# Optimization experiments

Hardware: AMD Instinct MI355X
Metric: run time of the kernel (lower is better)

## Reference

```python
import jax, jax.numpy as jnp
import numpy as np

WIN = 25            # window size (win_h == win_w == 25)
DIM = 256           # channels
DIM_HEAD = 32
HEADS = DIM // DIM_HEAD   # 8
HIDDEN = int(DIM * 2.0)   # mlp_ratio = 2.0
EPS = 1e-5


def _rel_pos_indices(w=WIN):
    # replicates the buffer built in Attention.__init__
    pos = np.arange(w)
    gi, gj = np.meshgrid(pos, pos, indexing='ij')
    grid = np.stack([gi.ravel(), gj.ravel()], axis=-1)          # (w*w, 2)
    rel = grid[:, None, :] - grid[None, :, :] + (w - 1)          # (n, n, 2)
    return jnp.asarray(rel[..., 0] * (2 * w - 1) + rel[..., 1])  # (n, n) int


def setup_inputs() -> dict:
    key = jax.random.key(0)
    ks = jax.random.split(key, 8)
    s = 0.02
    d = DIM
    return {
        'x': jax.random.normal(ks[0], (2, d, 100, 100), jnp.float32),
        'w_qkv': jax.random.normal(ks[1], (3 * d, d), jnp.float32) * s,
        'w_out': jax.random.normal(ks[2], (d, d), jnp.float32) * s,
        'rel_bias_table': jax.random.normal(ks[3], ((2 * WIN - 1) ** 2, HEADS), jnp.float32) * s,
        'gamma2': jnp.ones((d,), jnp.float32),
        'beta2': jnp.zeros((d,), jnp.float32),
        'w1': jax.random.normal(ks[4], (HIDDEN, d), jnp.float32) * s,
        'b1': jnp.zeros((HIDDEN,), jnp.float32),
        'w2': jax.random.normal(ks[5], (d, HIDDEN), jnp.float32) * s,
        'b2': jnp.zeros((d,), jnp.float32),
    }


def _layernorm(x, g, b, eps=EPS):
    m = x.mean(-1, keepdims=True)
    v = ((x - m) ** 2).mean(-1, keepdims=True)
    return (x - m) / jnp.sqrt(v + eps) * g + b


def reference(x, w_qkv, w_out, rel_bias_table, gamma2, beta2, w1, b1, w2, b2):
    b, d, H, W = x.shape
    nh, nw = H // WIN, W // WIN
    h, dh = HEADS, DIM_HEAD
    scale = dh ** -0.5
    n = WIN * WIN

    # --- window partition: (b, d, H, W) -> (b*nh*nw, n, d) ---
    xw = x.reshape(b, d, nh, WIN, nw, WIN).transpose(0, 2, 4, 3, 5, 1)
    xw = xw.reshape(b * nh * nw, n, d)

    # --- windowed attention with relative-position bias (norm1 unused in source) ---
    qkv = xw @ w_qkv.T                         # (B, n, 3d)
    q, k, v = jnp.split(qkv, 3, axis=-1)
    split_heads = lambda t: t.reshape(t.shape[0], n, h, dh).transpose(0, 2, 1, 3)
    q = split_heads(q) * scale                 # (B, h, n, dh)
    k = split_heads(k)
    v = split_heads(v)

    sim = jnp.einsum('bhid,bhjd->bhij', q, k)  # (B, h, n, n)
    bias = rel_bias_table[_rel_pos_indices()]  # (n, n, h)
    sim = sim + bias.transpose(2, 0, 1)[None]
    attn = jax.nn.softmax(sim, axis=-1)
    out = jnp.einsum('bhij,bhjd->bhid', attn, v)            # (B, h, n, dh)
    out = out.transpose(0, 2, 1, 3).reshape(-1, n, d)        # head-major concat: (m d)
    out = out @ w_out.T                                      # (B, n, d)

    # --- un-partition: (b*nh*nw, n, d) -> (b, d, H, W) ---
    xa = out.reshape(b, nh, nw, WIN, WIN, d).transpose(0, 5, 1, 3, 2, 4)
    xa = xa.reshape(b, d, H, W)

    # --- norm2 + MLP + residual ---
    y = xa.transpose(0, 2, 3, 1).reshape(b, H * W, d)
    y = _layernorm(y, gamma2, beta2)
    y = jax.nn.gelu(y @ w1.T + b1, approximate=False) @ w2.T + b2
    y = y.reshape(b, H, W, d).transpose(0, 3, 1, 2)
    return x + y
```

## Files before the change

kernel.cpp:

```cpp
#include <hip/hip_runtime.h>


using f32x4 = __attribute__((ext_vector_type(4))) float;
using s16x8 = __attribute__((ext_vector_type(8))) short;
using u32x4 = __attribute__((ext_vector_type(4))) unsigned;

__device__ __forceinline__ ushort f2b(float f) {
  union { float f; unsigned u; } v; v.f = f;
  return (ushort)((v.u + 0x7FFFu + ((v.u >> 16) & 1u)) >> 16);
}
__device__ __forceinline__ ushort f2b_fast(float f) {
  union { float f; unsigned u; } v; v.f = f;
  return (ushort)((v.u + 0x8000u) >> 16);
}
__device__ __forceinline__ float b2f(ushort u) {
  union { unsigned u; float f; } v; v.u = ((unsigned)u) << 16; return v.f;
}
__device__ __forceinline__ float lo2f(unsigned w) {
  union { unsigned u; float f; } v; v.u = w << 16; return v.f;
}
__device__ __forceinline__ float hi2f(unsigned w) {
  union { unsigned u; float f; } v; v.u = w & 0xffff0000u; return v.f;
}

__device__ __forceinline__ unsigned cvtpk(float lo, float hi) {
  unsigned r;
  asm("v_cvt_pk_bf16_f32 %0, %1, %2" : "=v"(r) : "v"(lo), "v"(hi));
  return r;
}
__device__ __forceinline__ void pl32(unsigned& a, unsigned& b) {
  asm("v_permlane32_swap_b32 %0, %1" : "+v"(a), "+v"(b));
}
__device__ __forceinline__ void pl16(unsigned& a, unsigned& b) {
  asm("v_permlane16_swap_b32 %0, %1" : "+v"(a), "+v"(b));
}

__device__ __forceinline__ void gld16(const void* g, void* l) {
  __builtin_amdgcn_global_load_lds((const __attribute__((address_space(1))) void*)g,
                                   (__attribute__((address_space(3))) void*)l, 16, 0, 0);
}

template<int KB, int WM, int WN, int MT, int NT>
__device__ __forceinline__ void gemm_core(const ushort* __restrict__ A, int lda,
                                          const ushort* __restrict__ B, int ldb,
                                          f32x4 acc[MT][NT]) {
  constexpr int TM = WM * MT * 16;
  constexpr int TN = WN * NT * 16;
  constexpr int NW = WM * WN;
  constexpr int RG = (TM + TN) / 8;
  static_assert(NW == 4 && RG % NW == 0 && TM % 8 == 0, "cfg");
  __shared__ ushort As[TM * 64];
  __shared__ ushort Bs[TN * 64];
  const int tid = threadIdx.x;
  const int lane = tid & 63;
  const int wv = tid >> 6;
  const int wr = (wv / WN) * (MT * 16);
  const int wc = (wv % WN) * (NT * 16);
  const int srow = lane >> 3;
  const int sg = ((lane & 7) ^ (srow & 7)) * 8;
  f32x4 zero = {0.f, 0.f, 0.f, 0.f};
#pragma unroll
  for (int mt = 0; mt < MT; ++mt)
#pragma unroll
    for (int nt = 0; nt < NT; ++nt) acc[mt][nt] = zero;

  for (int kb = 0; kb < KB; ++kb) {
#pragma unroll
    for (int i = 0; i < RG / NW; ++i) {
      int r0 = (i * NW + wv) * 8;
      if (r0 < TM) gld16(A + (r0 + srow) * lda + kb * 64 + sg, &As[r0 * 64]);
      else         gld16(B + (r0 - TM + srow) * ldb + kb * 64 + sg, &Bs[(r0 - TM) * 64]);
    }
    __syncthreads();
#pragma unroll
    for (int ks = 0; ks < 2; ++ks) {
      s16x8 af[MT], bfr[NT];
      const int G = ks * 4 + (lane >> 4);
#pragma unroll
      for (int mt = 0; mt < MT; ++mt) {
        int row = wr + mt * 16 + (lane & 15);
        af[mt] = *(const s16x8*)&As[row * 64 + (G ^ (row & 7)) * 8];
      }
#pragma unroll
      for (int nt = 0; nt < NT; ++nt) {
        int row = wc + nt * 16 + (lane & 15);
        bfr[nt] = *(const s16x8*)&Bs[row * 64 + (G ^ (row & 7)) * 8];
      }
#pragma unroll
      for (int mt = 0; mt < MT; ++mt)
#pragma unroll
        for (int nt = 0; nt < NT; ++nt)
          acc[mt][nt] = __builtin_amdgcn_mfma_f32_16x16x32_bf16(af[mt], bfr[nt], acc[mt][nt], 0, 0, 0);
    }
    __syncthreads();
  }
}

__global__ __launch_bounds__(256) void k_prep(const float* __restrict__ x,
                                              const float* __restrict__ wqkv,
                                              const float* __restrict__ wout,
                                              const float* __restrict__ w1,
                                              const float* __restrict__ w2,
                                              const float* __restrict__ table,
                                              ushort* __restrict__ Xw,
                                              ushort* __restrict__ wqkvb,
                                              ushort* __restrict__ woutb,
                                              ushort* __restrict__ w1b,
                                              ushort* __restrict__ w2b,
                                              ushort* __restrict__ biasPh) {
  __shared__ ushort smem[64 * 264];
  const int bid = blockIdx.x, tid = threadIdx.x;
  if (bid < 320) {
    ushort (*Ls)[264] = (ushort(*)[264])smem;
    const int t0 = bid * 64;
    const int w = t0 / 640;
    const int tokbase = t0 - w * 640;
    const int b = w >> 4, wh = (w >> 2) & 3, ww = w & 3;
    for (int i = tid; i < 64 * 256; i += 256) {
      int c = i >> 6, tl = i & 63;
      int tok = tokbase + tl;
      ushort val = 0;
      if (tok < 625) {
        int ii = tok / 25, jj = tok - ii * 25;
        val = f2b(x[((b * 256 + c) * 100 + wh * 25 + ii) * 100 + ww * 25 + jj]);
      }
      Ls[tl][c] = val;
    }
    __syncthreads();
    for (int i = tid; i < 64 * 32; i += 256) {
      int tl = i >> 5, g = (i & 31) * 8;
      *(uint4*)(Xw + (t0 + tl) * 256 + g) = *(const uint4*)&Ls[tl][g];
    }
  } else if (bid < 832) {
    int v = (bid - 320) * 1024 + tid * 4;
    const float* src; ushort* dst; int off;
    if (v < 196608)      { src = wqkv; dst = wqkvb; off = v; }
    else if (v < 262144) { src = wout; dst = woutb; off = v - 196608; }
    else if (v < 393216) { src = w1;   dst = w1b;   off = v - 262144; }
    else                 { src = w2;   dst = w2b;   off = v - 393216; }
    float4 f = *(const float4*)(src + off);
    ushort4 u; u.x = f2b(f.x); u.y = f2b(f.y); u.z = f2b(f.z); u.w = f2b(f.w);
    *(ushort4*)(dst + off) = u;
  } else {
    float* tl = (float*)smem;
    const int qb = bid - 832;
    const int h = qb / 40, t = qb - (qb / 40) * 40;
    for (int i = tid; i < 2401; i += 256) tl[i] = table[i * 8 + h] * 1.4426950408889634f;
    __syncthreads();
    const int lane = tid >> 2, rr = tid & 3;
    const int quad = lane >> 4, cl = lane & 15;
    int qrow = t * 16 + cl;
    int qg = (qrow < 625) ? qrow : 0;
    const int ri = qg / 25, ci = qg - ri * 25;
    for (int cc = 0; cc < 4; ++cc)
      for (int cp = 0; cp < 5; ++cp)
#pragma unroll
        for (int codd = 0; codd < 2; ++codd) {
          int kv = cc * 160 + (cp * 2 + codd) * 16 + quad * 4 + rr;
          float v = -1e30f;
          if (kv < 625) {
            int rj = kv / 25, cj = kv - rj * 25;
            v = tl[(ri - rj + 24) * 49 + (ci - cj + 24)];
          }
          biasPh[((((h * 40 + t) * 4 + cc) * 5 + cp) * 64 + lane) * 8 + codd * 4 + rr] = f2b(v);
        }
  }
}

__global__ __launch_bounds__(256) void k_qkv(const ushort* __restrict__ Xw,
                                             const ushort* __restrict__ Wb,
                                             ushort* __restrict__ Qb,
                                             ushort* __restrict__ Kb,
                                             ushort* __restrict__ VbT) {
  f32x4 acc[2][4];
  gemm_core<4, 2, 2, 2, 4>(Xw + blockIdx.x * 64 * 256, 256,
                           Wb + blockIdx.y * 128 * 256, 256, acc);
  const int lane = threadIdx.x & 63, wv = threadIdx.x >> 6;
  const int wr = (wv >> 1) * 32, wc = (wv & 1) * 64;
  const int which = blockIdx.y >> 1;
  const float QSC = 0.17677669529663687f * 1.4426950408889634f;
#pragma unroll
  for (int mt = 0; mt < 2; ++mt) {
#pragma unroll
    for (int nt = 0; nt < 4; ++nt) {
      int n = blockIdx.y * 128 + wc + nt * 16 + (lane & 15);
      int h = (n >> 5) & 7, ch = n & 31;
      int m0 = blockIdx.x * 64 + wr + mt * 16 + (lane >> 4) * 4;
      int w = m0 / 640, tok0 = m0 - w * 640;
      if (which == 2) {
        ushort4 pk;
        pk.x = f2b_fast(acc[mt][nt][0]); pk.y = f2b_fast(acc[mt][nt][1]);
        pk.z = f2b_fast(acc[mt][nt][2]); pk.w = f2b_fast(acc[mt][nt][3]);
        *(ushort4*)(VbT + (((w << 3) + h) * 32 + ch) * 640 + tok0) = pk;
      } else {
        ushort* dst = which == 0 ? Qb : Kb;
        float sc = which == 0 ? QSC : 1.f;
#pragma unroll
        for (int r = 0; r < 4; ++r)
          dst[(((w << 3) + h) * 640 + tok0 + r) * 32 + ch] = f2b_fast(acc[mt][nt][r] * sc);
      }
    }
  }
}

__global__ __launch_bounds__(128, 2) void k_attn(const ushort* __restrict__ Qb,
                                                 const ushort* __restrict__ Kb,
                                                 const ushort* __restrict__ VbT,
                                                 const ushort* __restrict__ biasPh,
                                                 ushort* __restrict__ AO) {
  const int tid = threadIdx.x;
  const int lane = tid & 63;
  const int wv = tid >> 6;
  const int quad = lane >> 4;
  const int cl = lane & 15;
  const int bid = blockIdx.x;
  const int h = bid & 7;
  const int rem = bid >> 3;
  const int win = rem / 5;
  const int tg = rem - win * 5;
  const ushort* Qg = Qb + (win * 8 + h) * 20480;
  const ushort* Kg = Kb + (win * 8 + h) * 20480;
  const ushort* Vt = VbT + (win * 8 + h) * 20480;

  const int t0 = tg * 8 + wv * 4;
  s16x8 qf[4];
#pragma unroll
  for (int tlp = 0; tlp < 4; ++tlp)
    qf[tlp] = *(const s16x8*)(Qg + ((t0 + tlp) * 16 + cl) * 32 + quad * 8);

  const f32x4 zero = {0.f, 0.f, 0.f, 0.f};
  f32x4 o0[4], o1[4];
  float ssum[4];
#pragma unroll
  for (int tlp = 0; tlp < 4; ++tlp) { o0[tlp] = zero; o1[tlp] = zero; ssum[tlp] = 0.f; }

  const ushort* bpB = biasPh + ((h * 40 + t0) * 20) * 512 + lane * 8;

  for (int ch2 = 0; ch2 < 10; ++ch2) {
    s16x8 kf[4], va[2], vb[2], bf2[8];
#pragma unroll
    for (int j = 0; j < 4; ++j)
      kf[j] = *(const s16x8*)(Kg + (ch2 * 64 + j * 16 + cl) * 32 + quad * 8);
#pragma unroll
    for (int j = 0; j < 2; ++j) {
      va[j] = *(const s16x8*)(Vt + cl * 640 + ch2 * 64 + j * 32 + quad * 8);
      vb[j] = *(const s16x8*)(Vt + (16 + cl) * 640 + ch2 * 64 + j * 32 + quad * 8);
    }
#pragma unroll
    for (int tlp = 0; tlp < 4; ++tlp) {
      bf2[tlp * 2]     = *(const s16x8*)(bpB + (tlp * 20 + 2 * ch2) * 512);
      bf2[tlp * 2 + 1] = *(const s16x8*)(bpB + (tlp * 20 + 2 * ch2 + 1) * 512);
    }
    __builtin_amdgcn_sched_barrier(0);
#pragma unroll
    for (int tlp = 0; tlp < 4; ++tlp) {
      const unsigned* w0 = (const unsigned*)&bf2[tlp * 2];
      const unsigned* w1 = (const unsigned*)&bf2[tlp * 2 + 1];
      f32x4 s0, s1, s2, s3;
      s0[0] = lo2f(w0[0]); s0[1] = hi2f(w0[0]); s0[2] = lo2f(w0[1]); s0[3] = hi2f(w0[1]);
      s1[0] = lo2f(w0[2]); s1[1] = hi2f(w0[2]); s1[2] = lo2f(w0[3]); s1[3] = hi2f(w0[3]);
      s2[0] = lo2f(w1[0]); s2[1] = hi2f(w1[0]); s2[2] = lo2f(w1[1]); s2[3] = hi2f(w1[1]);
      s3[0] = lo2f(w1[2]); s3[1] = hi2f(w1[2]); s3[2] = lo2f(w1[3]); s3[3] = hi2f(w1[3]);
      s0 = __builtin_amdgcn_mfma_f32_16x16x32_bf16(kf[0], qf[tlp], s0, 0, 0, 0);
      s1 = __builtin_amdgcn_mfma_f32_16x16x32_bf16(kf[1], qf[tlp], s1, 0, 0, 0);
      s2 = __builtin_amdgcn_mfma_f32_16x16x32_bf16(kf[2], qf[tlp], s2, 0, 0, 0);
      s3 = __builtin_amdgcn_mfma_f32_16x16x32_bf16(kf[3], qf[tlp], s3, 0, 0, 0);
#pragma unroll
      for (int r = 0; r < 4; ++r) {
        s0[r] = __builtin_amdgcn_exp2f(s0[r]);
        s1[r] = __builtin_amdgcn_exp2f(s1[r]);
        s2[r] = __builtin_amdgcn_exp2f(s2[r]);
        s3[r] = __builtin_amdgcn_exp2f(s3[r]);
      }
      ssum[tlp] += ((s0[0] + s0[1]) + (s0[2] + s0[3])) + ((s1[0] + s1[1]) + (s1[2] + s1[3]))
                 + ((s2[0] + s2[1]) + (s2[2] + s2[3])) + ((s3[0] + s3[1]) + (s3[2] + s3[3]));
      unsigned a0 = cvtpk(s0[0], s0[1]);
      unsigned a1 = cvtpk(s0[2], s0[3]);
      unsigned b0 = cvtpk(s1[0], s1[1]);
      unsigned b1 = cvtpk(s1[2], s1[3]);
      pl32(a0, b0); pl16(a0, b0);
      pl32(a1, b1); pl16(a1, b1);
      u32x4 pw0; pw0[0] = a0; pw0[1] = a1; pw0[2] = b0; pw0[3] = b1;
      s16x8 pf0 = __builtin_bit_cast(s16x8, pw0);
      o0[tlp] = __builtin_amdgcn_mfma_f32_16x16x32_bf16(va[0], pf0, o0[tlp], 0, 0, 0);
      o1[tlp] = __builtin_amdgcn_mfma_f32_16x16x32_bf16(vb[0], pf0, o1[tlp], 0, 0, 0);
      unsigned a2 = cvtpk(s2[0], s2[1]);
      unsigned a3 = cvtpk(s2[2], s2[3]);
      unsigned b2 = cvtpk(s3[0], s3[1]);
      unsigned b3 = cvtpk(s3[2], s3[3]);
      pl32(a2, b2); pl16(a2, b2);
      pl32(a3, b3); pl16(a3, b3);
      u32x4 pw1; pw1[0] = a2; pw1[1] = a3; pw1[2] = b2; pw1[3] = b3;
      s16x8 pf1 = __builtin_bit_cast(s16x8, pw1);
      o0[tlp] = __builtin_amdgcn_mfma_f32_16x16x32_bf16(va[1], pf1, o0[tlp], 0, 0, 0);
      o1[tlp] = __builtin_amdgcn_mfma_f32_16x16x32_bf16(vb[1], pf1, o1[tlp], 0, 0, 0);
    }
  }
#pragma unroll
  for (int tlp = 0; tlp < 4; ++tlp) {
    float s = ssum[tlp];
    unsigned ua = __builtin_bit_cast(unsigned, s), ub = ua;
    pl32(ua, ub);
    s = __builtin_bit_cast(float, ua) + __builtin_bit_cast(float, ub);
    ua = __builtin_bit_cast(unsigned, s); ub = ua;
    pl16(ua, ub);
    s = __builtin_bit_cast(float, ua) + __builtin_bit_cast(float, ub);
    int tok = (t0 + tlp) * 16 + cl;
    if (tok < 625) {
      float inv = 1.f / s;
      int base = (win * 640 + tok) * 256 + h * 32 + quad * 4;
      ushort4 p0, p1;
      p0.x = f2b_fast(o0[tlp][0] * inv); p0.y = f2b_fast(o0[tlp][1] * inv);
      p0.z = f2b_fast(o0[tlp][2] * inv); p0.w = f2b_fast(o0[tlp][3] * inv);
      p1.x = f2b_fast(o1[tlp][0] * inv); p1.y = f2b_fast(o1[tlp][1] * inv);
      p1.z = f2b_fast(o1[tlp][2] * inv); p1.w = f2b_fast(o1[tlp][3] * inv);
      *(ushort4*)(AO + base) = p0;
      *(ushort4*)(AO + base + 16) = p1;
    }
  }
}

__global__ __launch_bounds__(256) void k_out_ln(const ushort* __restrict__ AO,
                                                const ushort* __restrict__ Wb,
                                                const float* __restrict__ gamma,
                                                const float* __restrict__ beta,
                                                ushort* __restrict__ Yn) {
  __shared__ float red[4][32][2];
  f32x4 acc[2][4];
  gemm_core<4, 1, 4, 2, 4>(AO + blockIdx.x * 32 * 256, 256, Wb, 256, acc);
  const int tid = threadIdx.x;
  const int lane = tid & 63;
  const int wv = tid >> 6;
  const int wc = wv * 64;
  const int quad = lane >> 4, cl = lane & 15;
#pragma unroll
  for (int mt = 0; mt < 2; ++mt)
#pragma unroll
    for (int r = 0; r < 4; ++r) {
      float s = 0.f, ss = 0.f;
#pragma unroll
      for (int nt = 0; nt < 4; ++nt) { float v = acc[mt][nt][r]; s += v; ss += v * v; }
      s += __shfl_xor(s, 1, 64); ss += __shfl_xor(ss, 1, 64);
      s += __shfl_xor(s, 2, 64); ss += __shfl_xor(ss, 2, 64);
      s += __shfl_xor(s, 4, 64); ss += __shfl_xor(ss, 4, 64);
      s += __shfl_xor(s, 8, 64); ss += __shfl_xor(ss, 8, 64);
      if (cl == 0) {
        int row = mt * 16 + quad * 4 + r;
        red[wv][row][0] = s;
        red[wv][row][1] = ss;
      }
    }
  __syncthreads();
  float g[4], bt[4];
#pragma unroll
  for (int nt = 0; nt < 4; ++nt) { int n = wc + nt * 16 + cl; g[nt] = gamma[n]; bt[nt] = beta[n]; }
  const int m0 = blockIdx.x * 32;
#pragma unroll
  for (int mt = 0; mt < 2; ++mt)
#pragma unroll
    for (int r = 0; r < 4; ++r) {
      int row = mt * 16 + quad * 4 + r;
      int m = m0 + row;
      int w = m / 640, tok = m - w * 640;
      if (tok < 625) {
        float sum  = (red[0][row][0] + red[1][row][0]) + (red[2][row][0] + red[3][row][0]);
        float ssum = (red[0][row][1] + red[1][row][1]) + (red[2][row][1] + red[3][row][1]);
        float mean = sum * 0.00390625f;
        float var = ssum * 0.00390625f - mean * mean;
        float rstd = rsqrtf(var + 1e-5f);
        int b = w >> 4, whh = (w >> 2) & 3, www = w & 3;
        int ii = tok / 25, jj = tok - ii * 25;
        int p = (whh * 25 + ii) * 100 + www * 25 + jj;
        ushort* dst = Yn + (b * 10000 + p) * 256;
#pragma unroll
        for (int nt = 0; nt < 4; ++nt) {
          float v = (acc[mt][nt][r] - mean) * rstd * g[nt] + bt[nt];
          dst[wc + nt * 16 + cl] = f2b_fast(v);
        }
      }
    }
}

__global__ __launch_bounds__(256) void k_fc1(const ushort* __restrict__ Yn,
                                             const ushort* __restrict__ W1b,
                                             const float* __restrict__ b1,
                                             ushort* __restrict__ G) {
  f32x4 acc[2][4];
  gemm_core<4, 2, 2, 2, 4>(Yn + blockIdx.x * 64 * 256, 256,
                           W1b + blockIdx.y * 128 * 256, 256, acc);
  const int lane = threadIdx.x & 63, wv = threadIdx.x >> 6;
  const int wr = (wv >> 1) * 32, wc = (wv & 1) * 64;
#pragma unroll
  for (int mt = 0; mt < 2; ++mt)
#pragma unroll
    for (int nt = 0; nt < 4; ++nt) {
      int n = blockIdx.y * 128 + wc + nt * 16 + (lane & 15);
      float bias = b1[n];
#pragma unroll
      for (int r = 0; r < 4; ++r) {
        int m = blockIdx.x * 64 + wr + mt * 16 + (lane >> 4) * 4 + r;
        float v = acc[mt][nt][r] + bias;
        v = 0.5f * v * (1.f + erff(v * 0.70710678118f));
        G[m * 512 + n] = f2b_fast(v);
      }
    }
}

__global__ __launch_bounds__(256) void k_fc2(const ushort* __restrict__ W2b,
                                             const ushort* __restrict__ G,
                                             const float* __restrict__ b2,
                                             const float* __restrict__ x,
                                             float* __restrict__ out) {
  f32x4 acc[1][4];
  gemm_core<8, 2, 2, 1, 4>(W2b + blockIdx.x * 32 * 512, 512,
                           G + blockIdx.y * 128 * 512, 512, acc);
  const int lane = threadIdx.x & 63, wv = threadIdx.x >> 6;
  const int wr = (wv >> 1) * 16, wc = (wv & 1) * 64;
#pragma unroll
  for (int nt = 0; nt < 4; ++nt) {
    int t = blockIdx.y * 128 + wc + nt * 16 + (lane & 15);
    if (t < 20000) {
      int b = t / 10000, p = t - b * 10000;
#pragma unroll
      for (int r = 0; r < 4; ++r) {
        int c = blockIdx.x * 32 + wr + (lane >> 4) * 4 + r;
        int idx = (b * 256 + c) * 10000 + p;
        out[idx] = x[idx] + acc[0][nt][r] + b2[c];
      }
    }
  }
}

extern "C" void kernel_launch(void* const* d_in, const int* in_sizes, int n_in,
                              void* d_out, int out_size, void* d_ws, size_t ws_size,
                              hipStream_t stream) {
  const float* x     = (const float*)d_in[0];
  const float* wqkv  = (const float*)d_in[1];
  const float* wout  = (const float*)d_in[2];
  const float* bias  = (const float*)d_in[3];
  const float* gamma = (const float*)d_in[4];
  const float* beta  = (const float*)d_in[5];
  const float* w1    = (const float*)d_in[6];
  const float* b1    = (const float*)d_in[7];
  const float* w2    = (const float*)d_in[8];
  const float* b2    = (const float*)d_in[9];
  float* out = (float*)d_out;
  char* ws = (char*)d_ws;

  ushort* Xw    = (ushort*)(ws + 0);
  ushort* AO    = Xw;
  ushort* wqkvb = (ushort*)(ws + 10485760);
  ushort* woutb = (ushort*)(ws + 10878976);
  ushort* w1b   = (ushort*)(ws + 11010048);
  ushort* w2b   = (ushort*)(ws + 11272192);
  ushort* Qb    = (ushort*)(ws + 11534336);
  ushort* Kb    = (ushort*)(ws + 22020096);
  ushort* VbT   = (ushort*)(ws + 32505856);
  ushort* biasPh= (ushort*)(ws + 42991616);
  ushort* Yn    = (ushort*)(ws + 22020096);
  ushort* G     = (ushort*)(ws + 32505856);

  k_prep  <<<1152, 256, 0, stream>>>(x, wqkv, wout, w1, w2, bias,
                                     Xw, wqkvb, woutb, w1b, w2b, biasPh);
  k_qkv   <<<dim3(320, 6), 256, 0, stream>>>(Xw, wqkvb, Qb, Kb, VbT);
  k_attn  <<<1280, 128, 0, stream>>>(Qb, Kb, VbT, biasPh, AO);
  k_out_ln<<<640, 256, 0, stream>>>(AO, woutb, gamma, beta, Yn);
  k_fc1   <<<dim3(314, 4), 256, 0, stream>>>(Yn, w1b, b1, G);
  k_fc2   <<<dim3(8, 157), 256, 0, stream>>>(w2b, G, b2, x, out);
}
```

Before: 215.4 us.

## Fuse out-projection, LayerNorm, FC1+GELU and FC2 into one per-tile kernel

Replaces the separate out-proj+LN, fc1 and fc2 kernels with a single k_mlp kernel. Each block takes 32 tokens through all three GEMMs and keeps the intermediates (normalized activations and GELU output) in LDS in bf16 MFMA fragment layout, so the Yn and G tensors no longer round-trip through global memory. Weights are read straight from global/L2 per wave instead of being staged in LDS. In exchange the grid has only 640 blocks, the whole MLP is serialized per block, and register pressure is high (accumulators plus launch_bounds min 2), which can limit occupancy.

New measurement: 246.3 us. 14.3% more time.

```diff
diff --git a/kernel.cpp b/kernel.cpp
--- a/kernel.cpp
+++ b/kernel.cpp
@@ -12,9 +12,6 @@
 __device__ __forceinline__ ushort f2b_fast(float f) {
   union { float f; unsigned u; } v; v.f = f;
   return (ushort)((v.u + 0x8000u) >> 16);
-}
-__device__ __forceinline__ float b2f(ushort u) {
-  union { unsigned u; float f; } v; v.u = ((unsigned)u) << 16; return v.f;
 }
 __device__ __forceinline__ float lo2f(unsigned w) {
   union { unsigned u; float f; } v; v.u = w << 16; return v.f;
@@ -34,10 +31,29 @@
 __device__ __forceinline__ void pl16(unsigned& a, unsigned& b) {
   asm("v_permlane16_swap_b32 %0, %1" : "+v"(a), "+v"(b));
 }
+__device__ __forceinline__ float bfly4(float s) {
+  unsigned ua = __builtin_bit_cast(unsigned, s), ub = ua;
+  pl32(ua, ub);
+  s = __builtin_bit_cast(float, ua) + __builtin_bit_cast(float, ub);
+  ua = __builtin_bit_cast(unsigned, s); ub = ua;
+  pl16(ua, ub);
+  return __builtin_bit_cast(float, ua) + __builtin_bit_cast(float, ub);
+}
 
 __device__ __forceinline__ void gld16(const void* g, void* l) {
   __builtin_amdgcn_global_load_lds((const __attribute__((address_space(1))) void*)g,
                                    (__attribute__((address_space(3))) void*)l, 16, 0, 0);
+}
+
+__device__ __forceinline__ u32x4 xpose(const f32x4& s0, const f32x4& s1) {
+  unsigned a0 = cvtpk(s0[0], s0[1]);
+  unsigned a1 = cvtpk(s0[2], s0[3]);
+  unsigned b0 = cvtpk(s1[0], s1[1]);
+  unsigned b1 = cvtpk(s1[2], s1[3]);
+  pl32(a0, b0); pl16(a0, b0);
+  pl32(a1, b1); pl16(a1, b1);
+  u32x4 pw; pw[0] = a0; pw[1] = a1; pw[2] = b0; pw[3] = b1;
+  return pw;
 }
 
 template<int KB, int WM, int WN, int MT, int NT>
@@ -274,23 +290,11 @@
       }
       ssum[tlp] += ((s0[0] + s0[1]) + (s0[2] + s0[3])) + ((s1[0] + s1[1]) + (s1[2] + s1[3]))
                  + ((s2[0] + s2[1]) + (s2[2] + s2[3])) + ((s3[0] + s3[1]) + (s3[2] + s3[3]));
-      unsigned a0 = cvtpk(s0[0], s0[1]);
-      unsigned a1 = cvtpk(s0[2], s0[3]);
-      unsigned b0 = cvtpk(s1[0], s1[1]);
-      unsigned b1 = cvtpk(s1[2], s1[3]);
-      pl32(a0, b0); pl16(a0, b0);
-      pl32(a1, b1); pl16(a1, b1);
-      u32x4 pw0; pw0[0] = a0; pw0[1] = a1; pw0[2] = b0; pw0[3] = b1;
+      u32x4 pw0 = xpose(s0, s1);
       s16x8 pf0 = __builtin_bit_cast(s16x8, pw0);
       o0[tlp] = __builtin_amdgcn_mfma_f32_16x16x32_bf16(va[0], pf0, o0[tlp], 0, 0, 0);
       o1[tlp] = __builtin_amdgcn_mfma_f32_16x16x32_bf16(vb[0], pf0, o1[tlp], 0, 0, 0);
-      unsigned a2 = cvtpk(s2[0], s2[1]);
-      unsigned a3 = cvtpk(s2[2], s2[3]);
-      unsigned b2 = cvtpk(s3[0], s3[1]);
-      unsigned b3 = cvtpk(s3[2], s3[3]);
-      pl32(a2, b2); pl16(a2, b2);
-      pl32(a3, b3); pl16(a3, b3);
-      u32x4 pw1; pw1[0] = a2; pw1[1] = a3; pw1[2] = b2; pw1[3] = b3;
+      u32x4 pw1 = xpose(s2, s3);
       s16x8 pf1 = __builtin_bit_cast(s16x8, pw1);
       o0[tlp] = __builtin_amdgcn_mfma_f32_16x16x32_bf16(va[1], pf1, o0[tlp], 0, 0, 0);
       o1[tlp] = __builtin_amdgcn_mfma_f32_16x16x32_bf16(vb[1], pf1, o1[tlp], 0, 0, 0);
@@ -298,13 +302,7 @@
   }
 #pragma unroll
   for (int tlp = 0; tlp < 4; ++tlp) {
-    float s = ssum[tlp];
-    unsigned ua = __builtin_bit_cast(unsigned, s), ub = ua;
-    pl32(ua, ub);
-    s = __builtin_bit_cast(float, ua) + __builtin_bit_cast(float, ub);
-    ua = __builtin_bit_cast(unsigned, s); ub = ua;
-    pl16(ua, ub);
-    s = __builtin_bit_cast(float, ua) + __builtin_bit_cast(float, ub);
+    float s = bfly4(ssum[tlp]);
     int tok = (t0 + tlp) * 16 + cl;
     if (tok < 625) {
       float inv = 1.f / s;
@@ -320,113 +318,179 @@
   }
 }
 
-__global__ __launch_bounds__(256) void k_out_ln(const ushort* __restrict__ AO,
-                                                const ushort* __restrict__ Wb,
+__global__ __launch_bounds__(256, 2) void k_mlp(const ushort* __restrict__ AO,
+                                                const ushort* __restrict__ Wo,
                                                 const float* __restrict__ gamma,
                                                 const float* __restrict__ beta,
-                                                ushort* __restrict__ Yn) {
+                                                const ushort* __restrict__ W1b,
+                                                const float* __restrict__ b1,
+                                                const ushort* __restrict__ W2b,
+                                                const float* __restrict__ b2,
+                                                const float* __restrict__ x,
+                                                float* __restrict__ out) {
+  __shared__ ushort Bs1[32 * 64];
+  __shared__ ushort Ysf[8 * 2 * 64 * 8];
+  __shared__ ushort Gsf[16 * 2 * 64 * 8];
   __shared__ float red[4][32][2];
-  f32x4 acc[2][4];
-  gemm_core<4, 1, 4, 2, 4>(AO + blockIdx.x * 32 * 256, 256, Wb, 256, acc);
   const int tid = threadIdx.x;
   const int lane = tid & 63;
   const int wv = tid >> 6;
-  const int wc = wv * 64;
-  const int quad = lane >> 4, cl = lane & 15;
-#pragma unroll
-  for (int mt = 0; mt < 2; ++mt)
+  const int quad = lane >> 4;
+  const int cl = lane & 15;
+  const int m0 = blockIdx.x * 32;
+  const int srow = lane >> 3;
+  const int sg = ((lane & 7) ^ (srow & 7)) * 8;
+  const f32x4 zero = {0.f, 0.f, 0.f, 0.f};
+
+  f32x4 acc1[4][2];
+#pragma unroll
+  for (int mt = 0; mt < 4; ++mt)
+#pragma unroll
+    for (int ntk = 0; ntk < 2; ++ntk) acc1[mt][ntk] = zero;
+  for (int kb = 0; kb < 4; ++kb) {
+    int r0 = wv * 8;
+    gld16(AO + (m0 + r0 + srow) * 256 + kb * 64 + sg, &Bs1[r0 * 64]);
+    __syncthreads();
+#pragma unroll
+    for (int ks = 0; ks < 2; ++ks) {
+      const int G = ks * 4 + quad;
+      s16x8 bfr[2];
+#pragma unroll
+      for (int ntk = 0; ntk < 2; ++ntk) {
+        int row = ntk * 16 + cl;
+        bfr[ntk] = *(const s16x8*)&Bs1[row * 64 + (G ^ (row & 7)) * 8];
+      }
+#pragma unroll
+      for (int mt = 0; mt < 4; ++mt) {
+        s16x8 af = *(const s16x8*)(Wo + (wv * 64 + mt * 16 + cl) * 256 + kb * 64 + G * 8);
+#pragma unroll
+        for (int ntk = 0; ntk < 2; ++ntk)
+          acc1[mt][ntk] = __builtin_amdgcn_mfma_f32_16x16x32_bf16(af, bfr[ntk], acc1[mt][ntk], 0, 0, 0);
+      }
+    }
+    __syncthreads();
+  }
+#pragma unroll
+  for (int ntk = 0; ntk < 2; ++ntk) {
+    float s = 0.f, ss = 0.f;
+#pragma unroll
+    for (int mt = 0; mt < 4; ++mt)
+#pragma unroll
+      for (int r = 0; r < 4; ++r) { float v = acc1[mt][ntk][r]; s += v; ss += v * v; }
+    s = bfly4(s); ss = bfly4(ss);
+    if (quad == 0) { red[wv][ntk * 16 + cl][0] = s; red[wv][ntk * 16 + cl][1] = ss; }
+  }
+  __syncthreads();
+  float mean_[2], rstd_[2];
+#pragma unroll
+  for (int ntk = 0; ntk < 2; ++ntk) {
+    int i = ntk * 16 + cl;
+    float s  = (red[0][i][0] + red[1][i][0]) + (red[2][i][0] + red[3][i][0]);
+    float ss = (red[0][i][1] + red[1][i][1]) + (red[2][i][1] + red[3][i][1]);
+    float mean = s * 0.00390625f;
+    float var = ss * 0.00390625f - mean * mean;
+    mean_[ntk] = mean;
+    rstd_[ntk] = rsqrtf(var + 1e-5f);
+  }
+#pragma unroll
+  for (int mt = 0; mt < 4; ++mt) {
+    float gg[4], bb[4];
 #pragma unroll
     for (int r = 0; r < 4; ++r) {
-      float s = 0.f, ss = 0.f;
-#pragma unroll
-      for (int nt = 0; nt < 4; ++nt) { float v = acc[mt][nt][r]; s += v; ss += v * v; }
-      s += __shfl_xor(s, 1, 64); ss += __shfl_xor(ss, 1, 64);
-      s += __shfl_xor(s, 2, 64); ss += __shfl_xor(ss, 2, 64);
-      s += __shfl_xor(s, 4, 64); ss += __shfl_xor(ss, 4, 64);
-      s += __shfl_xor(s, 8, 64); ss += __shfl_xor(ss, 8, 64);
-      if (cl == 0) {
-        int row = mt * 16 + quad * 4 + r;
-        red[wv][row][0] = s;
-        red[wv][row][1] = ss;
-      }
+      int f = wv * 64 + mt * 16 + quad * 4 + r;
+      gg[r] = gamma[f]; bb[r] = beta[f];
+    }
+#pragma unroll
+    for (int ntk = 0; ntk < 2; ++ntk)
+#pragma unroll
+      for (int r = 0; r < 4; ++r)
+        acc1[mt][ntk][r] = (acc1[mt][ntk][r] - mean_[ntk]) * rstd_[ntk] * gg[r] + bb[r];
+  }
+#pragma unroll
+  for (int u = 0; u < 2; ++u)
+#pragma unroll
+    for (int ntk = 0; ntk < 2; ++ntk) {
+      u32x4 pw = xpose(acc1[2 * u][ntk], acc1[2 * u + 1][ntk]);
+      *(u32x4*)&Ysf[(((wv * 2 + u) * 2 + ntk) * 64 + lane) * 8] = pw;
     }
   __syncthreads();
-  float g[4], bt[4];
-#pragma unroll
-  for (int nt = 0; nt < 4; ++nt) { int n = wc + nt * 16 + cl; g[nt] = gamma[n]; bt[nt] = beta[n]; }
-  const int m0 = blockIdx.x * 32;
-#pragma unroll
-  for (int mt = 0; mt < 2; ++mt)
-#pragma unroll
-    for (int r = 0; r < 4; ++r) {
-      int row = mt * 16 + quad * 4 + r;
-      int m = m0 + row;
-      int w = m / 640, tok = m - w * 640;
-      if (tok < 625) {
-        float sum  = (red[0][row][0] + red[1][row][0]) + (red[2][row][0] + red[3][row][0]);
-        float ssum = (red[0][row][1] + red[1][row][1]) + (red[2][row][1] + red[3][row][1]);
-        float mean = sum * 0.00390625f;
-        float var = ssum * 0.00390625f - mean * mean;
-        float rstd = rsqrtf(var + 1e-5f);
-        int b = w >> 4, whh = (w >> 2) & 3, www = w & 3;
-        int ii = tok / 25, jj = tok - ii * 25;
-        int p = (whh * 25 + ii) * 100 + www * 25 + jj;
-        ushort* dst = Yn + (b * 10000 + p) * 256;
-#pragma unroll
-        for (int nt = 0; nt < 4; ++nt) {
-          float v = (acc[mt][nt][r] - mean) * rstd * g[nt] + bt[nt];
-          dst[wc + nt * 16 + cl] = f2b_fast(v);
+
+  f32x4 acc2[8][2];
+#pragma unroll
+  for (int mt = 0; mt < 8; ++mt)
+#pragma unroll
+    for (int ntk = 0; ntk < 2; ++ntk) acc2[mt][ntk] = zero;
+#pragma unroll
+  for (int c = 0; c < 8; ++c) {
+    s16x8 bfr[2];
+#pragma unroll
+    for (int ntk = 0; ntk < 2; ++ntk)
+      bfr[ntk] = *(const s16x8*)&Ysf[((c * 2 + ntk) * 64 + lane) * 8];
+#pragma unroll
+    for (int mt = 0; mt < 8; ++mt) {
+      s16x8 af = *(const s16x8*)(W1b + (wv * 128 + mt * 16 + cl) * 256 + c * 32 + quad * 8);
+#pragma unroll
+      for (int ntk = 0; ntk < 2; ++ntk)
+        acc2[mt][ntk] = __builtin_amdgcn_mfma_f32_16x16x32_bf16(af, bfr[ntk], acc2[mt][ntk], 0, 0, 0);
+    }
+  }
+#pragma unroll
+  for (int mt = 0; mt < 8; ++mt) {
+    float bb1[4];
+#pragma unroll
+    for (int r = 0; r < 4; ++r) bb1[r] = b1[wv * 128 + mt * 16 + quad * 4 + r];
+#pragma unroll
+    for (int ntk = 0; ntk < 2; ++ntk)
+#pragma unroll
+      for (int r = 0; r < 4; ++r) {
+        float v = acc2[mt][ntk][r] + bb1[r];
+        acc2[mt][ntk][r] = 0.5f * v * (1.f + erff(v * 0.70710678118f));
+      }
+  }
+#pragma unroll
+  for (int u = 0; u < 4; ++u)
+#pragma unroll
+    for (int ntk = 0; ntk < 2; ++ntk) {
+      u32x4 pw = xpose(acc2[2 * u][ntk], acc2[2 * u + 1][ntk]);
+      *(u32x4*)&Gsf[(((wv * 4 + u) * 2 + ntk) * 64 + lane) * 8] = pw;
+    }
+  __syncthreads();
+
+  f32x4 acc3[4][2];
+#pragma unroll
+  for (int mt = 0; mt < 4; ++mt)
+#pragma unroll
+    for (int ntk = 0; ntk < 2; ++ntk) acc3[mt][ntk] = zero;
+#pragma unroll
+  for (int c = 0; c < 16; ++c) {
+    s16x8 bfr[2];
+#pragma unroll
+    for (int ntk = 0; ntk < 2; ++ntk)
+      bfr[ntk] = *(const s16x8*)&Gsf[((c * 2 + ntk) * 64 + lane) * 8];
+#pragma unroll
+    for (int mt = 0; mt < 4; ++mt) {
+      s16x8 af = *(const s16x8*)(W2b + (wv * 64 + mt * 16 + cl) * 512 + c * 32 + quad * 8);
+#pragma unroll
+      for (int ntk = 0; ntk < 2; ++ntk)
+        acc3[mt][ntk] = __builtin_amdgcn_mfma_f32_16x16x32_bf16(af, bfr[ntk], acc3[mt][ntk], 0, 0, 0);
+    }
+  }
+#pragma unroll
+  for (int ntk = 0; ntk < 2; ++ntk) {
+    int m = m0 + ntk * 16 + cl;
+    int w = m / 640, tok = m - w * 640;
+    if (tok < 625) {
+      int b = w >> 4, whh = (w >> 2) & 3, www = w & 3;
+      int ii = tok / 25, jj = tok - ii * 25;
+      int p = (whh * 25 + ii) * 100 + www * 25 + jj;
+#pragma unroll
+      for (int mt = 0; mt < 4; ++mt)
+#pragma unroll
+        for (int r = 0; r < 4; ++r) {
+          int ch = wv * 64 + mt * 16 + quad * 4 + r;
+          int idx = (b * 256 + ch) * 10000 + p;
+          out[idx] = x[idx] + acc3[mt][ntk][r] + b2[ch];
         }
-      }
-    }
-}
-
-__global__ __launch_bounds__(256) void k_fc1(const ushort* __restrict__ Yn,
-                                             const ushort* __restrict__ W1b,
-                                             const float* __restrict__ b1,
-                                             ushort* __restrict__ G) {
-  f32x4 acc[2][4];
-  gemm_core<4, 2, 2, 2, 4>(Yn + blockIdx.x * 64 * 256, 256,
-                           W1b + blockIdx.y * 128 * 256, 256, acc);
-  const int lane = threadIdx.x & 63, wv = threadIdx.x >> 6;
-  const int wr = (wv >> 1) * 32, wc = (wv & 1) * 64;
-#pragma unroll
-  for (int mt = 0; mt < 2; ++mt)
-#pragma unroll
-    for (int nt = 0; nt < 4; ++nt) {
-      int n = blockIdx.y * 128 + wc + nt * 16 + (lane & 15);
-      float bias = b1[n];
-#pragma unroll
-      for (int r = 0; r < 4; ++r) {
-        int m = blockIdx.x * 64 + wr + mt * 16 + (lane >> 4) * 4 + r;
-        float v = acc[mt][nt][r] + bias;
-        v = 0.5f * v * (1.f + erff(v * 0.70710678118f));
-        G[m * 512 + n] = f2b_fast(v);
-      }
-    }
-}
-
-__global__ __launch_bounds__(256) void k_fc2(const ushort* __restrict__ W2b,
-                                             const ushort* __restrict__ G,
-                                             const float* __restrict__ b2,
-                                             const float* __restrict__ x,
-                                             float* __restrict__ out) {
-  f32x4 acc[1][4];
-  gemm_core<8, 2, 2, 1, 4>(W2b + blockIdx.x * 32 * 512, 512,
-                           G + blockIdx.y * 128 * 512, 512, acc);
-  const int lane = threadIdx.x & 63, wv = threadIdx.x >> 6;
-  const int wr = (wv >> 1) * 16, wc = (wv & 1) * 64;
-#pragma unroll
-  for (int nt = 0; nt < 4; ++nt) {
-    int t = blockIdx.y * 128 + wc + nt * 16 + (lane & 15);
-    if (t < 20000) {
-      int b = t / 10000, p = t - b * 10000;
-#pragma unroll
-      for (int r = 0; r < 4; ++r) {
-        int c = blockIdx.x * 32 + wr + (lane >> 4) * 4 + r;
-        int idx = (b * 256 + c) * 10000 + p;
-        out[idx] = x[idx] + acc[0][nt][r] + b2[c];
-      }
     }
   }
 }
@@ -457,14 +521,10 @@
   ushort* Kb    = (ushort*)(ws + 22020096);
   ushort* VbT   = (ushort*)(ws + 32505856);
   ushort* biasPh= (ushort*)(ws + 42991616);
-  ushort* Yn    = (ushort*)(ws + 22020096);
-  ushort* G     = (ushort*)(ws + 32505856);
-
-  k_prep  <<<1152, 256, 0, stream>>>(x, wqkv, wout, w1, w2, bias,
-                                     Xw, wqkvb, woutb, w1b, w2b, biasPh);
-  k_qkv   <<<dim3(320, 6), 256, 0, stream>>>(Xw, wqkvb, Qb, Kb, VbT);
-  k_attn  <<<1280, 128, 0, stream>>>(Qb, Kb, VbT, biasPh, AO);
-  k_out_ln<<<640, 256, 0, stream>>>(AO, woutb, gamma, beta, Yn);
-  k_fc1   <<<dim3(314, 4), 256, 0, stream>>>(Yn, w1b, b1, G);
-  k_fc2   <<<dim3(8, 157), 256, 0, stream>>>(w2b, G, b2, x, out);
-}
+
+  k_prep<<<1152, 256, 0, stream>>>(x, wqkv, wout, w1, w2, bias,
+                                   Xw, wqkvb, woutb, w1b, w2b, biasPh);
+  k_qkv <<<dim3(320, 6), 256, 0, stream>>>(Xw, wqkvb, Qb, Kb, VbT);
+  k_attn<<<1280, 128, 0, stream>>>(Qb, Kb, VbT, biasPh, AO);
+  k_mlp <<<640, 256, 0, stream>>>(AO, woutb, gamma, beta, w1b, b1, w2b, b2, x, out);
+}
```
